# Kernel tuning notes

Hardware: AMD Instinct MI355X
Metric: run time of the kernel (lower is better)

Reference implementation:

```python
import jax, jax.numpy as jnp
import numpy as np
import math

B, SEQ, E, H, NB, NHYP = 4, 1024, 512, 8, 64, 6
V, HID, NC, ENC = 32000, 2048, 6, 6
DH = E // H


def _pos_encoding(n, e, dtype):
    pos = jnp.arange(n, dtype=dtype)[:, None]
    div = jnp.exp(-jnp.arange(0, e, 2, dtype=dtype) * (math.log(10000.0) / e))
    ang = pos * div  # [n, e/2]
    pe = jnp.zeros((n, e), dtype)
    pe = pe.at[:, 0::2].set(jnp.sin(ang))
    pe = pe.at[:, 1::2].set(jnp.cos(ang))
    return pe


def _layer_norm(x, g, b):
    m = x.mean(-1, keepdims=True)
    v = ((x - m) ** 2).mean(-1, keepdims=True)
    return (x - m) / jnp.sqrt(v + 1e-5) * g + b


def _lsh_attention(x, Wq, bq, Wv, bv, hyper):
    b, n, e = x.shape
    q = x @ Wq + bq
    v = x @ Wv + bv
    q4 = q.reshape(b, n, H, DH)  # [b,n,h,d]
    v4 = v.reshape(b, n, H, DH)
    # bucket hashing: append bias 1, project on hyperplanes, binarize, binary-encode
    aug = jnp.concatenate([q4, jnp.ones((b, n, H, 1), q.dtype)], axis=-1)
    proj = jnp.einsum('bnhe,ey->bnhy', aug, hyper)
    bits = (proj >= 0).astype(q.dtype)
    pows = (2 ** jnp.arange(NHYP)).astype(q.dtype)
    buckets = jnp.einsum('bnhy,y->bnh', bits, pows).astype(jnp.int32)
    bh = buckets.transpose(0, 2, 1)  # [b,h,n]
    qh = q4.transpose(0, 2, 1, 3)  # [b,h,n,d]
    vh = v4.transpose(0, 2, 1, 3)
    scores = jnp.einsum('bhnd,bhmd->bhnm', qh, qh) / math.sqrt(e)
    # torch code zeroes q rows at their OWN bucket and sums q_c @ q_c^T over all
    # NB buckets; that equals scores * (NB - 2 + [bucket_i == bucket_j]) exactly.
    same = bh[:, :, :, None] == bh[:, :, None, :]
    count = (NB - 2 + same.astype(jnp.int32)).astype(scores.dtype)
    attn = jax.nn.softmax(scores * count, axis=-1)
    out = jnp.einsum('bhnm,bhmd->bhnd', attn, vh)
    return out.transpose(0, 2, 1, 3).reshape(b, n, e)


def setup_inputs() -> dict:
    key = jax.random.key(0)
    ks = jax.random.split(key, 16)
    s = 0.02
    emb = jax.random.normal(ks[0], (V, E), jnp.float32) * s
    emb = emb.at[V - 1].set(0.0)  # padding_idx row
    return dict(
        inputs=jax.random.randint(ks[1], (B, SEQ), 0, V),
        emb=emb,
        gamma=jnp.ones((E,), jnp.float32),
        beta=jnp.zeros((E,), jnp.float32),
        Wq=jax.random.normal(ks[2], (E, E), jnp.float32) * s,
        bq=jnp.zeros((E,), jnp.float32),
        Wv=jax.random.normal(ks[3], (E, E), jnp.float32) * s,
        bv=jnp.zeros((E,), jnp.float32),
        hyper=jax.random.normal(ks[4], (DH + 1, NHYP), jnp.float32),
        W1=jax.random.normal(ks[5], (E, HID), jnp.float32) * s,
        b1=jnp.zeros((HID,), jnp.float32),
        W2=jax.random.normal(ks[6], (HID, E), jnp.float32) * s,
        b2=jnp.zeros((E,), jnp.float32),
        Wm=jax.random.normal(ks[7], (E * SEQ, NC), jnp.float32) * 0.002,
        bm=jnp.zeros((NC,), jnp.float32),
    )


def reference(inputs, emb, gamma, beta, Wq, bq, Wv, bv, hyper, W1, b1, W2, b2, Wm, bm):
    x = emb[inputs]  # [B, SEQ, E]
    x = x + _pos_encoding(x.shape[1], x.shape[2], x.dtype)
    for _ in range(ENC):  # shared weights across encoders
        a = _lsh_attention(x, Wq, bq, Wv, bv, hyper)
        x = _layer_norm(a, gamma, beta)
        x = jax.nn.relu(x @ W1 + b1) @ W2 + b2 + x
        x = _layer_norm(x, gamma, beta)
    x = x.reshape(x.shape[0], -1)
    return x @ Wm + bm  # [B, NC]
```

## Files before the change

### kernel.cpp

```cpp
#include <hip/hip_runtime.h>
#include <hip/hip_bf16.h>
#include <math.h>

#define B_    4
#define SEQ_  1024
#define E_    512
#define H_    8
#define DH_   64
#define NHYP_ 6
#define HID_  2048
#define NC_   6
#define ENC_  6
#define BH_   (B_*H_)
#define NTOK_ 4096
#define NCAT_ 1088

typedef __attribute__((ext_vector_type(8))) short short8;
typedef __attribute__((ext_vector_type(4))) float f32x4;

static __device__ __forceinline__ float wave_rsum(float v){
#pragma unroll
  for(int o=32;o;o>>=1) v += __shfl_down(v,o,64);
  return v;
}
static __device__ __forceinline__ ushort f2b(float v){
  __hip_bfloat16 h = __float2bfloat16(v);
  return *(ushort*)&h;
}
static __device__ __forceinline__ float b2f(ushort u){
  unsigned int x = ((unsigned int)u) << 16;
  return *(float*)&x;
}
static __device__ __forceinline__ void gload16(const void* g, void* l){
  __builtin_amdgcn_global_load_lds(
      (const __attribute__((address_space(1))) void*)g,
      (__attribute__((address_space(3))) void*)l,
      16, 0, 0);
}

__global__ void embed_pe_kernel(const int* __restrict__ inp, const float* __restrict__ emb,
                                float* __restrict__ x, ushort* __restrict__ xh){
  int row = blockIdx.x;
  int s = row & (SEQ_-1);
  int idx = inp[row];
  const float* er = emb + (size_t)idx*E_;
  float* xr = x + (size_t)row*E_;
  ushort* hr = xh + (size_t)row*E_;
  for(int c=threadIdx.x;c<E_;c+=blockDim.x){
    int i = c>>1;
    float div = expf(-(float)i * 0.0359778920780319646f);
    float ang = (float)s * div;
    float pe = (c&1) ? cosf(ang) : sinf(ang);
    float v = er[c] + pe;
    xr[c] = v;
    hr[c] = f2b(v);
  }
}

__global__ __launch_bounds__(256) void transpose_cast(
    const float* __restrict__ W, ushort* __restrict__ Wt, int K, int N){
  __shared__ float T[32][33];
  int tx = threadIdx.x & 31, ty = threadIdx.x >> 5;
  int n0 = blockIdx.x*32, k0 = blockIdx.y*32;
#pragma unroll
  for(int i=0;i<32;i+=8) T[ty+i][tx] = W[(size_t)(k0+ty+i)*N + n0+tx];
  __syncthreads();
#pragma unroll
  for(int i=0;i<32;i+=8)
    Wt[(size_t)(n0+ty+i)*K + k0+tx] = f2b(T[tx][ty+i]);
}

__global__ void wproj_build(const float* __restrict__ Wq, const float* __restrict__ hyper,
                            ushort* __restrict__ WcatT){
  int t = blockIdx.x*256 + threadIdx.x;
  int c = t >> 9, k = t & 511;
  float s = 0.f;
  if(c < 48){
    int h = c/6, y = c%6;
    const float* wr = Wq + (size_t)k*E_ + h*DH_;
    for(int d=0;d<DH_;++d) s += wr[d]*hyper[d*NHYP_+y];
  }
  WcatT[(size_t)(1024+c)*E_ + k] = f2b(s);
}

__global__ void bias_build(const float* __restrict__ bq, const float* __restrict__ bv,
                           const float* __restrict__ hyper, float* __restrict__ bcat){
  int t = blockIdx.x*256 + threadIdx.x;
  if(t >= NCAT_) return;
  float v;
  if(t < 512) v = bq[t];
  else if(t < 1024) v = bv[t-512];
  else if(t < 1072){
    int c = t - 1024, h = c/6, y = c%6;
    float s = hyper[DH_*NHYP_ + y];
    for(int d=0;d<DH_;++d) s += bq[h*DH_+d]*hyper[d*NHYP_+y];
    v = s;
  } else v = 0.f;
  bcat[t] = v;
}

template<int BM, int BN, int EPI>
__global__ __launch_bounds__(256) void gemm_mfma(
    const ushort* __restrict__ A, const ushort* __restrict__ Bt,
    const float* __restrict__ bias, const float* __restrict__ res,
    void* __restrict__ C0, void* __restrict__ C1, void* __restrict__ C2,
    void* __restrict__ C3, int M, int N, int K)
{
  constexpr int MI = BM/32, NI = BN/32;
  constexpr int ACH = BM/32, BCH = BN/32;
  __shared__ ushort As[2][BM*64];
  __shared__ ushort Bs[2][BN*64];
  __shared__ float epi[64*49];
  int tid = threadIdx.x;
  int w = tid>>6, lane = tid&63, g = lane>>4, li = lane&15;
  int wr = w>>1, wc = w&1;
  int bm = blockIdx.y*BM, bn = blockIdx.x*BN;
  int kz = blockIdx.z;
  int kcnt = K / (int)gridDim.z;
  int kbase = kz * kcnt;
  int NK = kcnt >> 6;

  f32x4 acc[MI][NI] = {};

  auto issue = [&](int ks, int pb){
    int k0 = kbase + ks*64;
#pragma unroll
    for(int it=0; it<ACH; ++it){
      int c = it*256 + tid; int r = c>>3; int kq = ((c&7)^(r&7))*8;
      gload16(&A[(size_t)(bm+r)*K + k0 + kq], &As[pb][it*2048 + w*512]);
    }
#pragma unroll
    for(int it=0; it<BCH; ++it){
      int c = it*256 + tid; int r = c>>3; int kq = ((c&7)^(r&7))*8;
      gload16(&Bt[(size_t)(bn+r)*K + k0 + kq], &Bs[pb][it*2048 + w*512]);
    }
  };

  issue(0, 0);
  __syncthreads();
  for(int ks=0; ks<NK; ++ks){
    if(ks+1 < NK) issue(ks+1, (ks+1)&1);
    int pb = ks&1;
#pragma unroll
    for(int kc=0; kc<2; ++kc){
      short8 af[MI], bf[NI];
#pragma unroll
      for(int mi=0;mi<MI;++mi)
        af[mi] = *(const short8*)&As[pb][(wr*(BM/2)+mi*16+li)*64 + (((kc*4+g)^(li&7))*8)];
#pragma unroll
      for(int ni=0;ni<NI;++ni)
        bf[ni] = *(const short8*)&Bs[pb][(wc*(BN/2)+ni*16+li)*64 + (((kc*4+g)^(li&7))*8)];
#pragma unroll
      for(int mi=0;mi<MI;++mi)
#pragma unroll
        for(int ni=0;ni<NI;++ni)
          acc[mi][ni] = __builtin_amdgcn_mfma_f32_16x16x32_bf16(af[mi], bf[ni], acc[mi][ni], 0,0,0);
    }
    __syncthreads();
  }

  if(EPI==5){
    if(bn < 512){
      int h = bn >> 6;
#pragma unroll
      for(int mi=0;mi<MI;++mi){
        int rbase = bm + wr*(BM/2) + mi*16 + g*4;
        float q2s[4] = {0.f,0.f,0.f,0.f};
#pragma unroll
        for(int ni=0;ni<NI;++ni){
          int cc = bn + wc*(BN/2) + ni*16 + li;
          float bv = bias[cc];
          int d = cc & 63;
#pragma unroll
          for(int j=0;j<4;++j){
            float vvf = acc[mi][ni][j] + bv;
            ushort ub = f2b(vvf);
            int r = rbase + j; int b = r>>10, n = r&1023;
            ((ushort*)C1)[(((size_t)(b*8+h))*1024 + n)*64 + d] = ub;
            float f = b2f(ub);
            q2s[j] += f*f;
          }
        }
#pragma unroll
        for(int j=0;j<4;++j){
#pragma unroll
          for(int o=8;o;o>>=1) q2s[j] += __shfl_xor(q2s[j], o, 64);
        }
        if(li==0){
#pragma unroll
          for(int j=0;j<4;++j)
            epi[(wr*(BM/2)+mi*16+g*4+j)*2 + wc] = q2s[j];
        }
      }
      __syncthreads();
      if(tid < 64){
        int r = bm + tid; int b = r>>10, n = r&1023;
        ((float*)C3)[((size_t)(b*8+h))*1024 + n] = epi[tid*2] + epi[tid*2+1];
      }
    } else if(bn < 1024){
#pragma unroll
      for(int mi=0;mi<MI;++mi){
        int rbase = bm + wr*(BM/2) + mi*16 + g*4;
        int b = rbase>>10, n = rbase&1023;
#pragma unroll
        for(int ni=0;ni<NI;++ni){
          int cc = bn + wc*(BN/2) + ni*16 + li;
          float bv = bias[cc];
          int cl = cc - 512; int h = cl>>6, d = cl&63;
          ushort4 pk;
          pk.x = f2b(acc[mi][ni][0]+bv); pk.y = f2b(acc[mi][ni][1]+bv);
          pk.z = f2b(acc[mi][ni][2]+bv); pk.w = f2b(acc[mi][ni][3]+bv);
          *(ushort4*)&((ushort*)C2)[(((size_t)(b*8+h))*64 + d)*1024 + n] = pk;
        }
      }
    } else {
#pragma unroll
      for(int mi=0;mi<MI;++mi){
        int rloc = wr*(BM/2) + mi*16 + g*4;
#pragma unroll
        for(int ni=0;ni<NI;++ni){
          int c = wc*(BN/2) + ni*16 + li;
          if(c < 48){
            float bv = bias[1024 + c];
#pragma unroll
            for(int j=0;j<4;++j)
              epi[(rloc+j)*49 + c] = acc[mi][ni][j] + bv;
          }
        }
      }
      __syncthreads();
      if(tid < 64){
        int r = bm + tid; int b = r>>10, n = r&1023;
#pragma unroll
        for(int h=0;h<8;++h){
          int bk = 0;
#pragma unroll
          for(int y=0;y<NHYP_;++y)
            bk |= (epi[tid*49 + h*NHYP_ + y] >= 0.0f) ? (1<<y) : 0;
          ((int*)C0)[((size_t)(b*8+h))*1024 + n] = bk;
        }
      }
    }
    return;
  }

#pragma unroll
  for(int mi=0;mi<MI;++mi){
    int rbase = bm + wr*(BM/2) + mi*16 + g*4;
#pragma unroll
    for(int ni=0;ni<NI;++ni){
      int cc = bn + wc*(BN/2) + ni*16 + li;
      float bv = (EPI==6) ? 0.0f : bias[cc];
      float vv[4];
#pragma unroll
      for(int j=0;j<4;++j) vv[j] = acc[mi][ni][j] + bv;
      if(EPI==1){
#pragma unroll
        for(int j=0;j<4;++j) ((ushort*)C0)[(size_t)(rbase+j)*N + cc] = f2b(fmaxf(vv[j],0.0f));
      } else if(EPI==6){
        float* dst = (float*)C0 + (size_t)kz*M*N;
#pragma unroll
        for(int j=0;j<4;++j) dst[(size_t)(rbase+j)*N + cc] = vv[j];
      } else if(EPI==2){
#pragma unroll
        for(int j=0;j<4;++j){
          size_t o = (size_t)(rbase+j)*N + cc;
          ((float*)C0)[o] = vv[j] + res[o];
        }
      } else {
#pragma unroll
        for(int j=0;j<4;++j) ((float*)C0)[(size_t)(rbase+j)*N + cc] = vv[j];
      }
    }
  }
}

__global__ __launch_bounds__(256) void attn_mfma_kernel(
    const ushort* __restrict__ Qh,
    const ushort* __restrict__ Vt,
    const int* __restrict__ buckets,
    const float* __restrict__ qn2,
    float* __restrict__ outp)
{
  int bid = blockIdx.x;
  int bh = bid & 31;
  int qt = bid >> 5;
  int b = bh >> 3, h = bh & 7;
  int tid = threadIdx.x;
  int w = tid >> 6, lane = tid & 63;
  int g = lane >> 4, li = lane & 15;

  __shared__ ushort Ks[2][64*64];
  __shared__ ushort Vs[2][64*64];
  __shared__ ushort Ps[64*68];
  __shared__ int bks[2][64];
  __shared__ int bqs[64];
  __shared__ float mred[4];

  const ushort* Qbase = Qh + (size_t)bh*SEQ_*DH_;
  const ushort* Vbase = Vt + (size_t)bh*DH_*SEQ_;
  const int* Bb = buckets + bh*SEQ_;
  const float* qn = qn2 + bh*SEQ_;
  int q0 = qt*64;

  auto issue = [&](int kt, int pb){
    int j0 = kt*64;
#pragma unroll
    for(int it=0; it<2; ++it){
      int c = it*256 + tid; int r = c>>3; int ks = ((c&7)^(r&7))*8;
      gload16(&Qbase[(size_t)(j0+r)*DH_ + ks], &Ks[pb][it*2048 + w*512]);
      gload16(&Vbase[(size_t)r*SEQ_ + j0 + ks], &Vs[pb][it*2048 + w*512]);
    }
    if(tid < 16) gload16(&Bb[j0 + tid*4], &bks[pb][0]);
  };

  issue(0, 0);
  short8 qa[2];
  int qrow = q0 + w*16 + li;
#pragma unroll
  for(int kc=0; kc<2; ++kc)
    qa[kc] = *(const short8*)&Qbase[(size_t)qrow*DH_ + kc*32 + g*8];
  if(tid < 64) bqs[tid] = Bb[q0 + tid];

  float mx = 0.f;
  for(int i=tid;i<SEQ_;i+=256) mx = fmaxf(mx, qn[i]);
#pragma unroll
  for(int o=32;o;o>>=1) mx = fmaxf(mx, __shfl_xor(mx, o, 64));
  if(lane==0) mred[w] = mx;
  __syncthreads();
  float maxn = sqrtf(fmaxf(fmaxf(mred[0],mred[1]), fmaxf(mred[2],mred[3])));

  const float invsq = 0.04419417382415922f;
  const float c63 = invsq * 63.0f;
  float Mrow[4];
#pragma unroll
  for(int i=0;i<4;++i)
    Mrow[i] = c63 * sqrtf(qn[q0 + w*16 + g*4 + i]) * maxn + 1.0f;

  f32x4 acc_o[4] = {};
  float psum[4] = {0.f,0.f,0.f,0.f};

  for(int kt=0; kt<16; ++kt){
    if(kt < 15) issue(kt+1, (kt+1)&1);
    int pb = kt&1;

    f32x4 accs[4];
    __builtin_amdgcn_s_setprio(1);
#pragma unroll
    for(int nt=0; nt<4; ++nt){
      f32x4 z = {};
#pragma unroll
      for(int kc=0; kc<2; ++kc){
        short8 kb = *(const short8*)&Ks[pb][(nt*16+li)*64 + (((kc*4+g)^(li&7))*8)];
        z = __builtin_amdgcn_mfma_f32_16x16x32_bf16(qa[kc], kb, z, 0,0,0);
      }
      accs[nt] = z;
    }
    __builtin_amdgcn_s_setprio(0);
    int bkc[4];
#pragma unroll
    for(int nt=0;nt<4;++nt) bkc[nt] = bks[pb][nt*16 + li];

#pragma unroll
    for(int i=0;i<4;++i){
      int rloc = w*16 + g*4 + i;
      int bq = bqs[rloc];
      float rs = 0.f;
#pragma unroll
      for(int nt=0;nt<4;++nt){
        float cnt = (bkc[nt] == bq) ? 63.f : 62.f;
        float e = __expf(accs[nt][i] * (invsq * cnt) - Mrow[i]);
        rs += e;
        Ps[rloc*68 + nt*16 + li] = f2b(e);
      }
      psum[i] += rs;
    }
    __builtin_amdgcn_s_setprio(1);
#pragma unroll
    for(int dt=0; dt<4; ++dt){
      f32x4 z = acc_o[dt];
#pragma unroll
      for(int kc=0; kc<2; ++kc){
        short8 pa = *(const short8*)&Ps[(w*16+li)*68 + kc*32 + g*8];
        short8 vb = *(const short8*)&Vs[pb][(dt*16+li)*64 + (((kc*4+g)^(li&7))*8)];
        z = __builtin_amdgcn_mfma_f32_16x16x32_bf16(pa, vb, z, 0,0,0);
      }
      acc_o[dt] = z;
    }
    __builtin_amdgcn_s_setprio(0);
    __syncthreads();
  }
#pragma unroll
  for(int i=0;i<4;++i){
#pragma unroll
    for(int o=8;o;o>>=1) psum[i] += __shfl_xor(psum[i], o, 64);
  }
  float* obase = outp + ((size_t)(b*SEQ_ + q0 + w*16 + g*4))*E_ + h*DH_;
#pragma unroll
  for(int i=0;i<4;++i){
    float inv = 1.0f / fmaxf(psum[i], 1e-35f);
#pragma unroll
    for(int dt=0;dt<4;++dt)
      obase[(size_t)i*E_ + dt*16 + li] = acc_o[dt][i] * inv;
  }
}

__global__ __launch_bounds__(256) void ln_kernel(
    const float* __restrict__ in, const float* __restrict__ g,
    const float* __restrict__ bb, float* __restrict__ outp,
    ushort* __restrict__ oh){
  int row = blockIdx.x*4 + (threadIdx.x>>6);
  int lane = threadIdx.x & 63;
  const float4* xr = (const float4*)(in + (size_t)row*E_);
  float4 v0 = xr[lane*2], v1 = xr[lane*2+1];
  float s  = v0.x+v0.y+v0.z+v0.w + v1.x+v1.y+v1.z+v1.w;
  float s2 = v0.x*v0.x+v0.y*v0.y+v0.z*v0.z+v0.w*v0.w
           + v1.x*v1.x+v1.y*v1.y+v1.z*v1.z+v1.w*v1.w;
#pragma unroll
  for(int o=32;o;o>>=1){ s += __shfl_xor(s,o,64); s2 += __shfl_xor(s2,o,64); }
  float mean = s*(1.0f/E_);
  float var  = s2*(1.0f/E_) - mean*mean;
  float inv = rsqrtf(var + 1e-5f);
  const float4* g4 = (const float4*)(g) + lane*2;
  const float4* b4 = (const float4*)(bb) + lane*2;
  float4 g0 = g4[0], g1 = g4[1], b0 = b4[0], b1 = b4[1];
  float4 y0, y1;
  y0.x=(v0.x-mean)*inv*g0.x+b0.x; y0.y=(v0.y-mean)*inv*g0.y+b0.y;
  y0.z=(v0.z-mean)*inv*g0.z+b0.z; y0.w=(v0.w-mean)*inv*g0.w+b0.w;
  y1.x=(v1.x-mean)*inv*g1.x+b1.x; y1.y=(v1.y-mean)*inv*g1.y+b1.y;
  y1.z=(v1.z-mean)*inv*g1.z+b1.z; y1.w=(v1.w-mean)*inv*g1.w+b1.w;
  float4* orow = (float4*)(outp + (size_t)row*E_) + lane*2;
  orow[0] = y0; orow[1] = y1;
  ushort hs[8];
  hs[0]=f2b(y0.x); hs[1]=f2b(y0.y); hs[2]=f2b(y0.z); hs[3]=f2b(y0.w);
  hs[4]=f2b(y1.x); hs[5]=f2b(y1.y); hs[6]=f2b(y1.z); hs[7]=f2b(y1.w);
  *(uint4*)&oh[(size_t)row*E_ + lane*8] = *(uint4*)hs;
}

__global__ __launch_bounds__(256) void ln2_kernel(
    const float* __restrict__ P, const float* __restrict__ b2,
    const float* __restrict__ Xres, const float* __restrict__ g,
    const float* __restrict__ bb, float* __restrict__ outp,
    ushort* __restrict__ oh){
  int row = blockIdx.x*4 + (threadIdx.x>>6);
  int lane = threadIdx.x & 63;
  const float4* p0 = (const float4*)(P + (size_t)row*E_) + lane*2;
  const float4* p1 = (const float4*)(P + (size_t)NTOK_*E_ + (size_t)row*E_) + lane*2;
  const float4* xr = (const float4*)(Xres + (size_t)row*E_) + lane*2;
  const float4* c4 = (const float4*)(b2) + lane*2;
  float4 v0 = p0[0], v1 = p0[1], u0 = p1[0], u1 = p1[1];
  float4 x0 = xr[0], x1 = xr[1], cb0 = c4[0], cb1 = c4[1];
  v0.x += u0.x + cb0.x + x0.x; v0.y += u0.y + cb0.y + x0.y;
  v0.z += u0.z + cb0.z + x0.z; v0.w += u0.w + cb0.w + x0.w;
  v1.x += u1.x + cb1.x + x1.x; v1.y += u1.y + cb1.y + x1.y;
  v1.z += u1.z + cb1.z + x1.z; v1.w += u1.w + cb1.w + x1.w;
  float s  = v0.x+v0.y+v0.z+v0.w + v1.x+v1.y+v1.z+v1.w;
  float s2 = v0.x*v0.x+v0.y*v0.y+v0.z*v0.z+v0.w*v0.w
           + v1.x*v1.x+v1.y*v1.y+v1.z*v1.z+v1.w*v1.w;
#pragma unroll
  for(int o=32;o;o>>=1){ s += __shfl_xor(s,o,64); s2 += __shfl_xor(s2,o,64); }
  float mean = s*(1.0f/E_);
  float var  = s2*(1.0f/E_) - mean*mean;
  float inv = rsqrtf(var + 1e-5f);
  const float4* g4 = (const float4*)(g) + lane*2;
  const float4* b4 = (const float4*)(bb) + lane*2;
  float4 g0 = g4[0], g1 = g4[1], b0 = b4[0], b1 = b4[1];
  float4 y0, y1;
  y0.x=(v0.x-mean)*inv*g0.x+b0.x; y0.y=(v0.y-mean)*inv*g0.y+b0.y;
  y0.z=(v0.z-mean)*inv*g0.z+b0.z; y0.w=(v0.w-mean)*inv*g0.w+b0.w;
  y1.x=(v1.x-mean)*inv*g1.x+b1.x; y1.y=(v1.y-mean)*inv*g1.y+b1.y;
  y1.z=(v1.z-mean)*inv*g1.z+b1.z; y1.w=(v1.w-mean)*inv*g1.w+b1.w;
  float4* orow = (float4*)(outp + (size_t)row*E_) + lane*2;
  orow[0] = y0; orow[1] = y1;
  ushort hs[8];
  hs[0]=f2b(y0.x); hs[1]=f2b(y0.y); hs[2]=f2b(y0.z); hs[3]=f2b(y0.w);
  hs[4]=f2b(y1.x); hs[5]=f2b(y1.y); hs[6]=f2b(y1.z); hs[7]=f2b(y1.w);
  *(uint4*)&oh[(size_t)row*E_ + lane*8] = *(uint4*)hs;
}

__global__ void final_partial(const float* __restrict__ x, const float* __restrict__ Wm,
                              float* __restrict__ part){
  int b  = blockIdx.x >> 7;
  int ch = blockIdx.x & 127;
  const float* xb = x + (size_t)b*SEQ_*E_;
  int k0 = ch*4096;
  float acc[NC_] = {};
  for(int k=k0+threadIdx.x; k<k0+4096; k+=256){
    float xv = xb[k];
    const float* wrow = Wm + (size_t)k*NC_;
#pragma unroll
    for(int c=0;c<NC_;++c) acc[c] += xv*wrow[c];
  }
#pragma unroll
  for(int c=0;c<NC_;++c) acc[c] = wave_rsum(acc[c]);
  __shared__ float r[4][NC_];
  int w = threadIdx.x>>6, lane = threadIdx.x&63;
  if(lane==0){
#pragma unroll
    for(int c=0;c<NC_;++c) r[w][c] = acc[c];
  }
  __syncthreads();
  if(threadIdx.x==0){
#pragma unroll
    for(int c=0;c<NC_;++c)
      part[(size_t)blockIdx.x*NC_ + c] = r[0][c]+r[1][c]+r[2][c]+r[3][c];
  }
}

__global__ void final_reduce(const float* __restrict__ part, const float* __restrict__ bm,
                             float* __restrict__ out){
  int t = threadIdx.x;
  if(t >= B_*NC_) return;
  int b = t / NC_, c = t % NC_;
  float s = bm[c];
  for(int i=0;i<128;++i) s += part[(size_t)(b*128+i)*NC_ + c];
  out[t] = s;
}

extern "C" void kernel_launch(void* const* d_in, const int* in_sizes, int n_in,
                              void* d_out, int out_size, void* d_ws, size_t ws_size,
                              hipStream_t stream){
  const int*   inp   = (const int*)d_in[0];
  const float* emb   = (const float*)d_in[1];
  const float* gamma = (const float*)d_in[2];
  const float* beta  = (const float*)d_in[3];
  const float* Wq    = (const float*)d_in[4];
  const float* bq    = (const float*)d_in[5];
  const float* Wv    = (const float*)d_in[6];
  const float* bv    = (const float*)d_in[7];
  const float* hyper = (const float*)d_in[8];
  const float* W1    = (const float*)d_in[9];
  const float* b1    = (const float*)d_in[10];
  const float* W2    = (const float*)d_in[11];
  const float* b2    = (const float*)d_in[12];
  const float* Wm    = (const float*)d_in[13];
  const float* bm    = (const float*)d_in[14];
  float* out = (float*)d_out;

  char* ws = (char*)d_ws;
  size_t off = 0;
  auto alloc = [&](size_t bytes)->void*{
    void* p = ws + off; off += (bytes + 255) & ~(size_t)255; return p;
  };
  const size_t NTOK = (size_t)B_*SEQ_;
  float*  X    = (float*)alloc(NTOK*E_*sizeof(float));
  float*  A    = (float*)alloc(NTOK*E_*sizeof(float));
  float*  Op   = (float*)alloc((size_t)2*NTOK*E_*sizeof(float));
  ushort* Xh   = (ushort*)alloc(NTOK*E_*sizeof(ushort));
  ushort* Hh   = (ushort*)alloc(NTOK*HID_*sizeof(ushort));
  int*    Bk   = (int*)  alloc((size_t)BH_*SEQ_*sizeof(int));
  float*  Qn2  = (float*)alloc((size_t)BH_*SEQ_*sizeof(float));
  float*  Pp   = (float*)alloc((size_t)B_*128*NC_*sizeof(float));
  ushort* Qh   = (ushort*)alloc((size_t)BH_*SEQ_*DH_*sizeof(ushort));
  ushort* Vt   = (ushort*)alloc((size_t)BH_*DH_*SEQ_*sizeof(ushort));
  ushort* WcatT= (ushort*)alloc((size_t)NCAT_*E_*sizeof(ushort));
  ushort* W1T  = (ushort*)alloc((size_t)HID_*E_*sizeof(ushort));
  ushort* W2T  = (ushort*)alloc((size_t)E_*HID_*sizeof(ushort));
  float*  bcat = (float*)alloc(NCAT_*sizeof(float));
  (void)ws_size; (void)in_sizes; (void)n_in; (void)out_size;

  transpose_cast<<<dim3(E_/32,  E_/32),  256, 0, stream>>>(Wq, WcatT, E_, E_);
  transpose_cast<<<dim3(E_/32,  E_/32),  256, 0, stream>>>(Wv, WcatT + (size_t)512*E_, E_, E_);
  wproj_build<<<128, 256, 0, stream>>>(Wq, hyper, WcatT);
  transpose_cast<<<dim3(HID_/32,E_/32),  256, 0, stream>>>(W1, W1T, E_, HID_);
  transpose_cast<<<dim3(E_/32,  HID_/32),256, 0, stream>>>(W2, W2T, HID_, E_);
  bias_build<<<5, 256, 0, stream>>>(bq, bv, hyper, bcat);

  embed_pe_kernel<<<B_*SEQ_, 256, 0, stream>>>(inp, emb, X, Xh);

  dim3 gQV(NCAT_/64, (B_*SEQ_)/64);
  dim3 gF1(HID_/128, (B_*SEQ_)/128);
  dim3 gF2(E_/64,    (B_*SEQ_)/64, 2);
  for(int l=0;l<ENC_;++l){
    gemm_mfma<64,64,5><<<gQV, 256, 0, stream>>>(Xh, WcatT, bcat, nullptr, Bk, Qh, Vt, Qn2, B_*SEQ_, NCAT_, E_);
    attn_mfma_kernel<<<BH_*16, 256, 0, stream>>>(Qh, Vt, Bk, Qn2, A);
    ln_kernel<<<B_*SEQ_/4, 256, 0, stream>>>(A, gamma, beta, X, Xh);
    gemm_mfma<128,128,1><<<gF1, 256, 0, stream>>>(Xh, W1T, b1, nullptr, Hh, nullptr, nullptr, nullptr, B_*SEQ_, HID_, E_);
    gemm_mfma<64,64,6><<<gF2, 256, 0, stream>>>(Hh, W2T, b2, nullptr, Op, nullptr, nullptr, nullptr, B_*SEQ_, E_, HID_);
    ln2_kernel<<<B_*SEQ_/4, 256, 0, stream>>>(Op, b2, X, gamma, beta, X, Xh);
  }
  final_partial<<<B_*128, 256, 0, stream>>>(X, Wm, Pp);
  final_reduce<<<1, 32, 0, stream>>>(Pp, bm, out);
}
```

Before: 588.4 us.

## Split attention key range across two blocks and combine in layer norm

Each attention block now processes only half of the key tiles, doubling the grid from 512 to 1024 blocks. Partial unnormalized outputs and row sums are written separately and merged in a new combine_ln kernel that also performs the layer norm. The exponent is rewritten as exp2 with a fused multiply-add, and the weight-prep launches are merged into a single kernel. This trades extra global traffic for partial outputs against better GPU occupancy, since 512 blocks underfill the device.

After: 606.7 us, median of 2. 1.03x slower.

```diff
diff --git a/kernel.cpp b/kernel.cpp
--- a/kernel.cpp
+++ b/kernel.cpp
@@ -57,46 +57,55 @@
   }
 }
 
-__global__ __launch_bounds__(256) void transpose_cast(
-    const float* __restrict__ W, ushort* __restrict__ Wt, int K, int N){
-  __shared__ float T[32][33];
-  int tx = threadIdx.x & 31, ty = threadIdx.x >> 5;
-  int n0 = blockIdx.x*32, k0 = blockIdx.y*32;
-#pragma unroll
-  for(int i=0;i<32;i+=8) T[ty+i][tx] = W[(size_t)(k0+ty+i)*N + n0+tx];
-  __syncthreads();
-#pragma unroll
-  for(int i=0;i<32;i+=8)
-    Wt[(size_t)(n0+ty+i)*K + k0+tx] = f2b(T[tx][ty+i]);
-}
-
-__global__ void wproj_build(const float* __restrict__ Wq, const float* __restrict__ hyper,
-                            ushort* __restrict__ WcatT){
-  int t = blockIdx.x*256 + threadIdx.x;
-  int c = t >> 9, k = t & 511;
-  float s = 0.f;
-  if(c < 48){
-    int h = c/6, y = c%6;
-    const float* wr = Wq + (size_t)k*E_ + h*DH_;
-    for(int d=0;d<DH_;++d) s += wr[d]*hyper[d*NHYP_+y];
-  }
-  WcatT[(size_t)(1024+c)*E_ + k] = f2b(s);
-}
-
-__global__ void bias_build(const float* __restrict__ bq, const float* __restrict__ bv,
-                           const float* __restrict__ hyper, float* __restrict__ bcat){
-  int t = blockIdx.x*256 + threadIdx.x;
-  if(t >= NCAT_) return;
-  float v;
-  if(t < 512) v = bq[t];
-  else if(t < 1024) v = bv[t-512];
-  else if(t < 1072){
-    int c = t - 1024, h = c/6, y = c%6;
-    float s = hyper[DH_*NHYP_ + y];
-    for(int d=0;d<DH_;++d) s += bq[h*DH_+d]*hyper[d*NHYP_+y];
-    v = s;
-  } else v = 0.f;
-  bcat[t] = v;
+__global__ __launch_bounds__(256) void prep_kernel(
+    const float* __restrict__ Wq, const float* __restrict__ Wv,
+    const float* __restrict__ W1, const float* __restrict__ W2,
+    const float* __restrict__ bq, const float* __restrict__ bv,
+    const float* __restrict__ hyper,
+    ushort* __restrict__ WcatT, ushort* __restrict__ W1T,
+    ushort* __restrict__ W2T, float* __restrict__ bcat)
+{
+  int bid = blockIdx.x;
+  if(bid < 2560){
+    const float* W; ushort* Wt; int K, N, tile;
+    if(bid < 256){       W=Wq; Wt=WcatT;                    K=512;  N=512;  tile=bid; }
+    else if(bid < 512){  W=Wv; Wt=WcatT+(size_t)512*512;    K=512;  N=512;  tile=bid-256; }
+    else if(bid < 1536){ W=W1; Wt=W1T;                      K=512;  N=2048; tile=bid-512; }
+    else {               W=W2; Wt=W2T;                      K=2048; N=512;  tile=bid-1536; }
+    int tpr = N >> 5;
+    int n0 = (tile % tpr)*32, k0 = (tile / tpr)*32;
+    __shared__ float T[32][33];
+    int tx = threadIdx.x & 31, ty = threadIdx.x >> 5;
+#pragma unroll
+    for(int i=0;i<32;i+=8) T[ty+i][tx] = W[(size_t)(k0+ty+i)*N + n0+tx];
+    __syncthreads();
+#pragma unroll
+    for(int i=0;i<32;i+=8)
+      Wt[(size_t)(n0+ty+i)*K + k0+tx] = f2b(T[tx][ty+i]);
+  } else if(bid < 2688){
+    int t = (bid-2560)*256 + threadIdx.x;
+    int c = t >> 9, k = t & 511;
+    float s = 0.f;
+    if(c < 48){
+      int h = c/6, y = c%6;
+      const float* wr = Wq + (size_t)k*E_ + h*DH_;
+      for(int d=0;d<DH_;++d) s += wr[d]*hyper[d*NHYP_+y];
+    }
+    WcatT[(size_t)(1024+c)*E_ + k] = f2b(s);
+  } else {
+    int t = (bid-2688)*256 + threadIdx.x;
+    if(t >= NCAT_) return;
+    float v;
+    if(t < 512) v = bq[t];
+    else if(t < 1024) v = bv[t-512];
+    else if(t < 1072){
+      int c = t - 1024, h = c/6, y = c%6;
+      float s = hyper[DH_*NHYP_ + y];
+      for(int d=0;d<DH_;++d) s += bq[h*DH_+d]*hyper[d*NHYP_+y];
+      v = s;
+    } else v = 0.f;
+    bcat[t] = v;
+  }
 }
 
 template<int BM, int BN, int EPI>
@@ -280,11 +289,13 @@
     const ushort* __restrict__ Vt,
     const int* __restrict__ buckets,
     const float* __restrict__ qn2,
-    float* __restrict__ outp)
+    float* __restrict__ Op,
+    float* __restrict__ Sp)
 {
   int bid = blockIdx.x;
-  int bh = bid & 31;
-  int qt = bid >> 5;
+  int bh   = bid & 31;
+  int half = (bid >> 5) & 1;
+  int qt   = bid >> 6;
   int b = bh >> 3, h = bh & 7;
   int tid = threadIdx.x;
   int w = tid >> 6, lane = tid & 63;
@@ -302,6 +313,7 @@
   const int* Bb = buckets + bh*SEQ_;
   const float* qn = qn2 + bh*SEQ_;
   int q0 = qt*64;
+  int kt0 = half*8;
 
   auto issue = [&](int kt, int pb){
     int j0 = kt*64;
@@ -314,7 +326,7 @@
     if(tid < 16) gload16(&Bb[j0 + tid*4], &bks[pb][0]);
   };
 
-  issue(0, 0);
+  issue(kt0, 0);
   short8 qa[2];
   int qrow = q0 + w*16 + li;
 #pragma unroll
@@ -331,18 +343,23 @@
   float maxn = sqrtf(fmaxf(fmaxf(mred[0],mred[1]), fmaxf(mred[2],mred[3])));
 
   const float invsq = 0.04419417382415922f;
-  const float c63 = invsq * 63.0f;
-  float Mrow[4];
-#pragma unroll
-  for(int i=0;i<4;++i)
-    Mrow[i] = c63 * sqrtf(qn[q0 + w*16 + g*4 + i]) * maxn + 1.0f;
+  const float LOG2E = 1.4426950408889634f;
+  const float c62l = invsq * 62.0f * LOG2E;
+  const float c63l = invsq * 63.0f * LOG2E;
+  float nM2[4];
+#pragma unroll
+  for(int i=0;i<4;++i){
+    float Mrow = invsq*63.0f * sqrtf(qn[q0 + w*16 + g*4 + i]) * maxn + 1.0f;
+    nM2[i] = -Mrow * LOG2E;
+  }
 
   f32x4 acc_o[4] = {};
   float psum[4] = {0.f,0.f,0.f,0.f};
 
-  for(int kt=0; kt<16; ++kt){
-    if(kt < 15) issue(kt+1, (kt+1)&1);
-    int pb = kt&1;
+  for(int t=0; t<8; ++t){
+    int kt = kt0 + t;
+    if(t < 7) issue(kt+1, (t+1)&1);
+    int pb = t&1;
 
     f32x4 accs[4];
     __builtin_amdgcn_s_setprio(1);
@@ -368,8 +385,8 @@
       float rs = 0.f;
 #pragma unroll
       for(int nt=0;nt<4;++nt){
-        float cnt = (bkc[nt] == bq) ? 63.f : 62.f;
-        float e = __expf(accs[nt][i] * (invsq * cnt) - Mrow[i]);
+        float cl = (bkc[nt] == bq) ? c63l : c62l;
+        float e = exp2f(fmaf(accs[nt][i], cl, nM2[i]));
         rs += e;
         Ps[rloc*68 + nt*16 + li] = f2b(e);
       }
@@ -395,24 +412,37 @@
 #pragma unroll
     for(int o=8;o;o>>=1) psum[i] += __shfl_xor(psum[i], o, 64);
   }
-  float* obase = outp + ((size_t)(b*SEQ_ + q0 + w*16 + g*4))*E_ + h*DH_;
+  float* obase = Op + (size_t)half*NTOK_*E_
+               + ((size_t)(b*SEQ_ + q0 + w*16 + g*4))*E_ + h*DH_;
 #pragma unroll
   for(int i=0;i<4;++i){
-    float inv = 1.0f / fmaxf(psum[i], 1e-35f);
 #pragma unroll
     for(int dt=0;dt<4;++dt)
-      obase[(size_t)i*E_ + dt*16 + li] = acc_o[dt][i] * inv;
-  }
-}
-
-__global__ __launch_bounds__(256) void ln_kernel(
-    const float* __restrict__ in, const float* __restrict__ g,
-    const float* __restrict__ bb, float* __restrict__ outp,
-    ushort* __restrict__ oh){
+      obase[(size_t)i*E_ + dt*16 + li] = acc_o[dt][i];
+  }
+  if(li == 0){
+    float* sp = Sp + (size_t)half*BH_*SEQ_ + (size_t)bh*SEQ_ + q0 + w*16 + g*4;
+#pragma unroll
+    for(int i=0;i<4;++i) sp[i] = psum[i];
+  }
+}
+
+__global__ __launch_bounds__(256) void combine_ln(
+    const float* __restrict__ Op, const float* __restrict__ Sp,
+    const float* __restrict__ g, const float* __restrict__ bb,
+    float* __restrict__ outp, ushort* __restrict__ oh){
   int row = blockIdx.x*4 + (threadIdx.x>>6);
   int lane = threadIdx.x & 63;
-  const float4* xr = (const float4*)(in + (size_t)row*E_);
-  float4 v0 = xr[lane*2], v1 = xr[lane*2+1];
+  int b = row >> 10, n = row & 1023;
+  int h = lane >> 3;
+  size_t sidx = (size_t)(b*8+h)*SEQ_ + n;
+  float ps = Sp[sidx] + Sp[(size_t)BH_*SEQ_ + sidx];
+  float inv0 = 1.0f / fmaxf(ps, 1e-35f);
+  const float4* o1 = (const float4*)(Op + (size_t)row*E_) + lane*2;
+  const float4* o2 = (const float4*)(Op + (size_t)NTOK_*E_ + (size_t)row*E_) + lane*2;
+  float4 v0 = o1[0], v1 = o1[1], u0 = o2[0], u1 = o2[1];
+  v0.x=(v0.x+u0.x)*inv0; v0.y=(v0.y+u0.y)*inv0; v0.z=(v0.z+u0.z)*inv0; v0.w=(v0.w+u0.w)*inv0;
+  v1.x=(v1.x+u1.x)*inv0; v1.y=(v1.y+u1.y)*inv0; v1.z=(v1.z+u1.z)*inv0; v1.w=(v1.w+u1.w)*inv0;
   float s  = v0.x+v0.y+v0.z+v0.w + v1.x+v1.y+v1.z+v1.w;
   float s2 = v0.x*v0.x+v0.y*v0.y+v0.z*v0.z+v0.w*v0.w
            + v1.x*v1.x+v1.y*v1.y+v1.z*v1.z+v1.w*v1.w;
@@ -544,8 +574,8 @@
   };
   const size_t NTOK = (size_t)B_*SEQ_;
   float*  X    = (float*)alloc(NTOK*E_*sizeof(float));
-  float*  A    = (float*)alloc(NTOK*E_*sizeof(float));
   float*  Op   = (float*)alloc((size_t)2*NTOK*E_*sizeof(float));
+  float*  Sp   = (float*)alloc((size_t)2*BH_*SEQ_*sizeof(float));
   ushort* Xh   = (ushort*)alloc(NTOK*E_*sizeof(ushort));
   ushort* Hh   = (ushort*)alloc(NTOK*HID_*sizeof(ushort));
   int*    Bk   = (int*)  alloc((size_t)BH_*SEQ_*sizeof(int));
@@ -559,13 +589,8 @@
   float*  bcat = (float*)alloc(NCAT_*sizeof(float));
   (void)ws_size; (void)in_sizes; (void)n_in; (void)out_size;
 
-  transpose_cast<<<dim3(E_/32,  E_/32),  256, 0, stream>>>(Wq, WcatT, E_, E_);
-  transpose_cast<<<dim3(E_/32,  E_/32),  256, 0, stream>>>(Wv, WcatT + (size_t)512*E_, E_, E_);
-  wproj_build<<<128, 256, 0, stream>>>(Wq, hyper, WcatT);
-  transpose_cast<<<dim3(HID_/32,E_/32),  256, 0, stream>>>(W1, W1T, E_, HID_);
-  transpose_cast<<<dim3(E_/32,  HID_/32),256, 0, stream>>>(W2, W2T, HID_, E_);
-  bias_build<<<5, 256, 0, stream>>>(bq, bv, hyper, bcat);
-
+  prep_kernel<<<2693, 256, 0, stream>>>(Wq, Wv, W1, W2, bq, bv, hyper,
+                                        WcatT, W1T, W2T, bcat);
   embed_pe_kernel<<<B_*SEQ_, 256, 0, stream>>>(inp, emb, X, Xh);
 
   dim3 gQV(NCAT_/64, (B_*SEQ_)/64);
@@ -573,8 +598,8 @@
   dim3 gF2(E_/64,    (B_*SEQ_)/64, 2);
   for(int l=0;l<ENC_;++l){
     gemm_mfma<64,64,5><<<gQV, 256, 0, stream>>>(Xh, WcatT, bcat, nullptr, Bk, Qh, Vt, Qn2, B_*SEQ_, NCAT_, E_);
-    attn_mfma_kernel<<<BH_*16, 256, 0, stream>>>(Qh, Vt, Bk, Qn2, A);
-    ln_kernel<<<B_*SEQ_/4, 256, 0, stream>>>(A, gamma, beta, X, Xh);
+    attn_mfma_kernel<<<BH_*32, 256, 0, stream>>>(Qh, Vt, Bk, Qn2, Op, Sp);
+    combine_ln<<<B_*SEQ_/4, 256, 0, stream>>>(Op, Sp, gamma, beta, X, Xh);
     gemm_mfma<128,128,1><<<gF1, 256, 0, stream>>>(Xh, W1T, b1, nullptr, Hh, nullptr, nullptr, nullptr, B_*SEQ_, HID_, E_);
     gemm_mfma<64,64,6><<<gF2, 256, 0, stream>>>(Hh, W2T, b2, nullptr, Op, nullptr, nullptr, nullptr, B_*SEQ_, E_, HID_);
     ln2_kernel<<<B_*SEQ_/4, 256, 0, stream>>>(Op, b2, X, gamma, beta, X, Xh);
```
